# Kernel optimization log

Measured on AMD Instinct MI355X. Metric: run time of the kernel, lower is better.

## Reference

```python
import jax, jax.numpy as jnp
import numpy as np

EMBED = 768
HIDDEN = 3072
HEADS = 12
EPS = 1e-6


def _ln(x, g, b):
    mu = jnp.mean(x, axis=-1, keepdims=True)
    var = jnp.mean(jnp.square(x - mu), axis=-1, keepdims=True)
    return (x - mu) / jnp.sqrt(var + EPS) * g + b


def setup_inputs() -> dict:
    key = jax.random.key(0)
    ks = jax.random.split(key, 12)
    s = lambda fan_in: 1.0 / np.sqrt(fan_in)
    x = jax.random.normal(ks[0], (16, 1024, EMBED), dtype=jnp.float32)
    return {
        "x": x,
        "ln1_g": jnp.ones((EMBED,), jnp.float32),
        "ln1_b": jnp.zeros((EMBED,), jnp.float32),
        "qkv_w": jax.random.uniform(ks[1], (3 * EMBED, EMBED), jnp.float32, -s(EMBED), s(EMBED)),
        "qkv_b": jax.random.uniform(ks[2], (3 * EMBED,), jnp.float32, -s(EMBED), s(EMBED)),
        "proj_w": jax.random.uniform(ks[3], (EMBED, EMBED), jnp.float32, -s(EMBED), s(EMBED)),
        "proj_b": jax.random.uniform(ks[4], (EMBED,), jnp.float32, -s(EMBED), s(EMBED)),
        "ln2_g": jnp.ones((EMBED,), jnp.float32),
        "ln2_b": jnp.zeros((EMBED,), jnp.float32),
        "fc1_w": jax.random.uniform(ks[5], (HIDDEN, EMBED), jnp.float32, -s(EMBED), s(EMBED)),
        "fc1_b": jax.random.uniform(ks[6], (HIDDEN,), jnp.float32, -s(EMBED), s(EMBED)),
        "fc2_w": jax.random.uniform(ks[7], (EMBED, HIDDEN), jnp.float32, -s(HIDDEN), s(HIDDEN)),
        "fc2_b": jax.random.uniform(ks[8], (EMBED,), jnp.float32, -s(HIDDEN), s(HIDDEN)),
    }


def reference(x, ln1_g, ln1_b, qkv_w, qkv_b, proj_w, proj_b, ln2_g, ln2_b, fc1_w, fc1_b, fc2_w, fc2_b):
    B, N, D = x.shape
    Hd = D // HEADS
    scale = Hd ** -0.5
    # attention branch
    xn = _ln(x, ln1_g, ln1_b)
    qkv = xn @ qkv_w.T + qkv_b  # [B,N,3D]
    qkv = qkv.reshape(B, N, 3, HEADS, Hd).transpose(2, 0, 3, 1, 4)
    q, k, v = qkv[0], qkv[1], qkv[2]  # [B,H,N,Hd]
    attn = jax.nn.softmax(jnp.einsum("bhqd,bhkd->bhqk", q, k) * scale, axis=-1)
    ctx = jnp.einsum("bhqk,bhkd->bhqd", attn, v)
    ctx = ctx.transpose(0, 2, 1, 3).reshape(B, N, D)
    x = x + ctx @ proj_w.T + proj_b
    # MLP branch
    h = _ln(x, ln2_g, ln2_b)
    h = jax.nn.gelu(h @ fc1_w.T + fc1_b, approximate=False)
    x = x + h @ fc2_w.T + fc2_b
    return x
```

## Files before the change

kernel.cpp:

```cpp
#include <hip/hip_runtime.h>
#include <math.h>


typedef unsigned short u16;
typedef __attribute__((ext_vector_type(8))) short bf16x8;
typedef __attribute__((ext_vector_type(4))) float f32x4;

#define MFMA_BF16(a, b, c) __builtin_amdgcn_mfma_f32_16x16x32_bf16((a), (b), (c), 0, 0, 0)
#define MEMFENCE asm volatile("" ::: "memory")
#define WAITV(N) asm volatile("s_waitcnt vmcnt(" #N ")" ::: "memory")
#define WAITLGKM0 asm volatile("s_waitcnt lgkmcnt(0)" ::: "memory")
#define SCHED0 __builtin_amdgcn_sched_barrier(0)
#define EXP2F(x) __builtin_amdgcn_exp2f(x)

#define QSCALE 0.18033688011112042f
#define C8LOG2E 11.541560327111707f

__device__ __forceinline__ float bf2f(u16 v) {
    return __uint_as_float(((unsigned)v) << 16);
}
__device__ __forceinline__ u16 f2bf(float f) {
    unsigned u = __float_as_uint(f);
    u += 0x7fffu + ((u >> 16) & 1u);
    return (u16)(u >> 16);
}
__device__ __forceinline__ unsigned cvtpk_bf16(float lo, float hi) {
    unsigned r;
    asm volatile("v_cvt_pk_bf16_f32 %0, %1, %2" : "=v"(r) : "v"(lo), "v"(hi));
    return r;
}

__device__ __forceinline__ float gelu_fast(float v) {
    const float t = v * v;
    const float z = v * (1.5957691216f + 0.0713548162f * t);
    const float e = __expf(-z);
    return v * __builtin_amdgcn_rcpf(1.0f + e);
}

typedef __attribute__((address_space(1))) const void gvoid;
typedef __attribute__((address_space(3))) void lvoid;
__device__ __forceinline__ void gll16(const void* g, void* l) {
    __builtin_amdgcn_global_load_lds((gvoid*)g, (lvoid*)l, 16, 0, 0);
}

__global__ __launch_bounds__(256) void cast32(const float* __restrict__ src,
                                              u16* __restrict__ dst, int n8) {
    const int i = blockIdx.x * 256 + threadIdx.x;
    if (i >= n8) return;
    const float4 a = ((const float4*)src)[2 * i];
    const float4 b = ((const float4*)src)[2 * i + 1];
    bf16x8 r;
    r[0] = (short)f2bf(a.x); r[1] = (short)f2bf(a.y);
    r[2] = (short)f2bf(a.z); r[3] = (short)f2bf(a.w);
    r[4] = (short)f2bf(b.x); r[5] = (short)f2bf(b.y);
    r[6] = (short)f2bf(b.z); r[7] = (short)f2bf(b.w);
    ((bf16x8*)dst)[i] = r;
}

__global__ __launch_bounds__(256) void ln_kernel(const float* __restrict__ x,
                                                 const float* __restrict__ g,
                                                 const float* __restrict__ b,
                                                 u16* __restrict__ out) {
    const int row = blockIdx.x;
    const int t = threadIdx.x;
    const float* xr = x + (size_t)row * 768;
    float v0 = xr[t], v1 = xr[t + 256], v2 = xr[t + 512];
    float s = v0 + v1 + v2;
    float sq = v0 * v0 + v1 * v1 + v2 * v2;
#pragma unroll
    for (int off = 32; off > 0; off >>= 1) {
        s += __shfl_down(s, off);
        sq += __shfl_down(sq, off);
    }
    __shared__ float red_s[4], red_sq[4], sh_mu, sh_rs;
    const int wave = t >> 6, lane = t & 63;
    if (lane == 0) { red_s[wave] = s; red_sq[wave] = sq; }
    __syncthreads();
    if (t == 0) {
        float S = red_s[0] + red_s[1] + red_s[2] + red_s[3];
        float SQ = red_sq[0] + red_sq[1] + red_sq[2] + red_sq[3];
        float mu = S * (1.0f / 768.0f);
        float var = SQ * (1.0f / 768.0f) - mu * mu;
        sh_mu = mu;
        sh_rs = 1.0f / sqrtf(fmaxf(var, 0.0f) + 1e-6f);
    }
    __syncthreads();
    const float mu = sh_mu, rs = sh_rs;
    u16* orow = out + (size_t)row * 768;
    orow[t]       = f2bf((v0 - mu) * rs * g[t]       + b[t]);
    orow[t + 256] = f2bf((v1 - mu) * rs * g[t + 256] + b[t + 256]);
    orow[t + 512] = f2bf((v2 - mu) * rs * g[t + 512] + b[t + 512]);
}

template <int EPI, int BF16B>
__global__ __launch_bounds__(256, 2) void gemm2(
        const u16* __restrict__ A, const void* __restrict__ Bv,
        const float* __restrict__ bias, const float* __restrict__ res,
        void* __restrict__ Cv, u16* __restrict__ vtb, int N, int K) {
    __shared__ __align__(16) u16 As[128 * 32];
    __shared__ __align__(16) u16 Bs[128 * 32];
    const int t = threadIdx.x;
    const int wave = t >> 6, lane = t & 63;
    const int quad = lane >> 4, mr = lane & 15;
    const int wm = wave >> 1, wn = wave & 1;
    const int m0 = blockIdx.y * 128;
    const int n0 = blockIdx.x * 128;

    f32x4 acc[4][4];
#pragma unroll
    for (int i = 0; i < 4; i++)
#pragma unroll
        for (int j = 0; j < 4; j++) acc[i][j] = (f32x4){0.f, 0.f, 0.f, 0.f};

    const int seg = wave * 2;
    const int drow = lane >> 2;
    const int dcol = (lane & 3) * 8;
    const int sr = t >> 2, skv = t & 3;

    for (int k0 = 0; k0 < K; k0 += 32) {
#pragma unroll
        for (int c = 0; c < 2; c++) {
            const int rowA = (seg + c) * 16 + drow;
            gll16(A + (size_t)(m0 + rowA) * K + k0 + dcol, &As[(seg + c) * 512]);
        }
        if (BF16B) {
            const u16* Bh = (const u16*)Bv;
#pragma unroll
            for (int c = 0; c < 2; c++) {
                const int rowB = (seg + c) * 16 + drow;
                gll16(Bh + (size_t)(n0 + rowB) * K + k0 + dcol, &Bs[(seg + c) * 512]);
            }
        } else {
            const float* Bf = (const float*)Bv;
#pragma unroll
            for (int half = 0; half < 2; half++) {
                const float* src = Bf + (size_t)(n0 + sr + half * 64) * K + k0 + skv * 8;
                const float4 a = *(const float4*)src;
                const float4 b2 = *(const float4*)(src + 4);
                bf16x8 r;
                r[0] = (short)f2bf(a.x);  r[1] = (short)f2bf(a.y);
                r[2] = (short)f2bf(a.z);  r[3] = (short)f2bf(a.w);
                r[4] = (short)f2bf(b2.x); r[5] = (short)f2bf(b2.y);
                r[6] = (short)f2bf(b2.z); r[7] = (short)f2bf(b2.w);
                *(bf16x8*)&Bs[(sr + half * 64) * 32 + skv * 8] = r;
            }
        }
        __syncthreads();
        bf16x8 af[4], bfr[4];
#pragma unroll
        for (int i = 0; i < 4; i++)
            af[i] = *(const bf16x8*)&As[(wm * 64 + i * 16 + mr) * 32 + quad * 8];
#pragma unroll
        for (int j = 0; j < 4; j++)
            bfr[j] = *(const bf16x8*)&Bs[(wn * 64 + j * 16 + mr) * 32 + quad * 8];
#pragma unroll
        for (int i = 0; i < 4; i++)
#pragma unroll
            for (int j = 0; j < 4; j++)
                acc[i][j] = MFMA_BF16(af[i], bfr[j], acc[i][j]);
        __syncthreads();
    }

#pragma unroll
    for (int i = 0; i < 4; i++) {
#pragma unroll
        for (int r = 0; r < 4; r++) {
            const int m = m0 + wm * 64 + i * 16 + quad * 4 + r;
#pragma unroll
            for (int j = 0; j < 4; j++) {
                const int n = n0 + wn * 64 + j * 16 + mr;
                float v = acc[i][j][r] + bias[n];
                if (EPI == 1) {
                    v = gelu_fast(v);
                    ((u16*)Cv)[(size_t)m * N + n] = f2bf(v);
                } else if (EPI == 2) {
                    v += res[(size_t)m * N + n];
                    ((float*)Cv)[(size_t)m * N + n] = v;
                } else {
                    if (n < 1536) {
                        const float vq = (n < 768) ? v * QSCALE : v;
                        ((u16*)Cv)[(size_t)m * 1536 + n] = f2bf(vq);
                    } else {
                        const int h = (n - 1536) >> 6, hd = (n - 1536) & 63;
                        const int bb = m >> 10, pos = m & 1023;
                        vtb[((size_t)(bb * 12 + h) * 64 + hd) * 1024 + pos] = f2bf(v);
                    }
                }
            }
        }
    }
}

#define AFRAG(T, ROW, KS) \
    (*(const bf16x8*)&(T)[(ROW)][(((((KS) << 2) | quad)) ^ ((ROW) & 7)) << 3])

#define ACCUM(ACCEL, AF, BF)                                  \
    do {                                                      \
        if (EPI == 3) (ACCEL) = MFMA_BF16((AF), (BF), (ACCEL)); \
        else          (ACCEL) = MFMA_BF16((BF), (AF), (ACCEL)); \
    } while (0)

template <int EPI>
__global__ __launch_bounds__(512, 2) void gemm8(
        const u16* __restrict__ A, const u16* __restrict__ Bw,
        const float* __restrict__ bias, const float* __restrict__ res,
        void* __restrict__ Cv, u16* __restrict__ vtb, int N, int K) {
    __shared__ __align__(16) u16 SMEM[4][256][64];
    u16(&As)[2][256][64] = *reinterpret_cast<u16(*)[2][256][64]>(&SMEM[0][0][0]);
    u16(&Bs)[2][256][64] = *reinterpret_cast<u16(*)[2][256][64]>(&SMEM[2][0][0]);
    const int t = threadIdx.x;
    const int wave = t >> 6, lane = t & 63;
    const int quad = lane >> 4, mr = lane & 15;
    const int wm = wave >> 2, wn = wave & 3;
    const int gx = gridDim.x;
    const int nwg = gx * gridDim.y;
    int bid = blockIdx.y * gx + blockIdx.x;
    bid = (bid & 7) * (nwg >> 3) + (bid >> 3);
    const int m0 = (bid / gx) * 256, n0 = (bid % gx) * 256;
    const int NT = K >> 6;

    const int srow = wave * 8 + (lane >> 3);
    const int sgrp = ((lane & 7) ^ (lane >> 3)) * 8;

    const u16* Abase = A + (size_t)(m0 + srow) * K + sgrp;
    const u16* Bbase = Bw + (size_t)(n0 + srow) * K + sgrp;

#define STAGE_A(BI, SLOT, KT) \
    gll16(Abase + ((size_t)(SLOT) * 64) * K + (KT) * 64, &As[BI][(SLOT) * 64 + wave * 8][0])
#define STAGE_B(BI, SLOT, KT) \
    gll16(Bbase + ((size_t)(SLOT) * 64) * K + (KT) * 64, &Bs[BI][(SLOT) * 64 + wave * 8][0])

    STAGE_A(0, 0, 0); STAGE_A(0, 1, 0); STAGE_A(0, 2, 0); STAGE_A(0, 3, 0);
    STAGE_B(0, 0, 0); STAGE_B(0, 1, 0); STAGE_B(0, 2, 0); STAGE_B(0, 3, 0);
    if (NT > 1) { STAGE_A(1, 0, 1); STAGE_A(1, 2, 1); STAGE_B(1, 0, 1); STAGE_B(1, 1, 1); }

    f32x4 acc[8][4];
#pragma unroll
    for (int i = 0; i < 8; i++)
#pragma unroll
        for (int j = 0; j < 4; j++) acc[i][j] = (f32x4){0.f, 0.f, 0.f, 0.f};

    if (NT > 1) { WAITV(4); } else { WAITV(0); }
    __builtin_amdgcn_s_barrier();
    SCHED0;

    for (int kt = 0; kt < NT; ++kt) {
        const int bi = kt & 1;
        const u16(*Ab)[64] = As[bi];
        const u16(*Bb)[64] = Bs[bi];
        const bool st1 = (kt + 1 < NT);
        const bool st2 = (kt + 2 < NT);

        if (st1) { STAGE_B(bi ^ 1, 2, kt + 1); STAGE_B(bi ^ 1, 3, kt + 1);
                   STAGE_A(bi ^ 1, 1, kt + 1); STAGE_A(bi ^ 1, 3, kt + 1); }

        bf16x8 af[4], bfv[4];
#pragma unroll
        for (int j = 0; j < 4; j++) bfv[j] = AFRAG(Bb, wn * 64 + j * 16 + mr, 0);
#pragma unroll
        for (int i = 0; i < 4; i++) af[i] = AFRAG(Ab, wm * 128 + i * 16 + mr, 0);
#pragma unroll
        for (int i = 0; i < 4; i++)
#pragma unroll
            for (int j = 0; j < 4; j++) ACCUM(acc[i][j], af[i], bfv[j]);
#pragma unroll
        for (int i = 0; i < 4; i++) af[i] = AFRAG(Ab, wm * 128 + 64 + i * 16 + mr, 0);
#pragma unroll
        for (int i = 0; i < 4; i++)
#pragma unroll
            for (int j = 0; j < 4; j++) ACCUM(acc[4 + i][j], af[i], bfv[j]);
#pragma unroll
        for (int j = 0; j < 4; j++) bfv[j] = AFRAG(Bb, wn * 64 + j * 16 + mr, 1);
#pragma unroll
        for (int i = 0; i < 4; i++) af[i] = AFRAG(Ab, wm * 128 + i * 16 + mr, 1);
#pragma unroll
        for (int i = 0; i < 4; i++)
#pragma unroll
            for (int j = 0; j < 4; j++) ACCUM(acc[i][j], af[i], bfv[j]);
#pragma unroll
        for (int i = 0; i < 4; i++) af[i] = AFRAG(Ab, wm * 128 + 64 + i * 16 + mr, 1);
#pragma unroll
        for (int i = 0; i < 4; i++)
#pragma unroll
            for (int j = 0; j < 4; j++) ACCUM(acc[4 + i][j], af[i], bfv[j]);

        WAITLGKM0;
        SCHED0;
        __builtin_amdgcn_s_barrier();
        SCHED0;
        if (st2) { STAGE_A(bi, 0, kt + 2); STAGE_A(bi, 2, kt + 2);
                   STAGE_B(bi, 0, kt + 2); STAGE_B(bi, 1, kt + 2); }
        SCHED0;
        if (st2) { WAITV(4); } else { WAITV(0); }
        __builtin_amdgcn_s_barrier();
        SCHED0;
    }

    if (EPI == 3) {
        if (n0 >= 1536) {
            u16* Ls = &SMEM[0][0][0];
            __syncthreads();
#pragma unroll
            for (int i = 0; i < 8; i++) {
                const int mbase = wm * 128 + i * 16 + quad * 4;
                const int mch = mbase >> 3, mlo = mbase & 7;
#pragma unroll
                for (int j = 0; j < 4; j++) {
                    const int nl = wn * 64 + j * 16 + mr;
                    float v0 = acc[i][j][0] + bias[n0 + nl];
                    float v1 = acc[i][j][1] + bias[n0 + nl];
                    float v2 = acc[i][j][2] + bias[n0 + nl];
                    float v3 = acc[i][j][3] + bias[n0 + nl];
                    ushort4 w;
                    w.x = f2bf(v0); w.y = f2bf(v1); w.z = f2bf(v2); w.w = f2bf(v3);
                    *(ushort4*)(Ls + nl * 256 + ((mch ^ (nl & 7)) << 3) + mlo) = w;
                }
            }
            __syncthreads();
            const int bb = m0 >> 10, pos0 = m0 & 1023;
#pragma unroll
            for (int it = 0; it < 32; it++) {
                const int nl = it * 8 + wave;
                const int h = (n0 - 1536 + nl) >> 6;
                const int hd = nl & 63;
                const int mch = (lane >> 1) ^ (nl & 7);
                const ushort4 v =
                    *(const ushort4*)(Ls + nl * 256 + (mch << 3) + (lane & 1) * 4);
                u16* dst = vtb + ((size_t)(bb * 12 + h) * 64 + hd) * 1024 + pos0 + lane * 4;
                *(ushort4*)dst = v;
            }
        } else {
#pragma unroll
            for (int i = 0; i < 8; i++) {
#pragma unroll
                for (int r = 0; r < 4; r++) {
                    const int m = m0 + wm * 128 + (i >> 2) * 64 + (i & 3) * 16 + quad * 4 + r;
#pragma unroll
                    for (int j = 0; j < 4; j++) {
                        const int n = n0 + wn * 64 + j * 16 + mr;
                        float v = acc[i][j][r] + bias[n];
                        const float vq = (n < 768) ? v * QSCALE : v;
                        ((u16*)Cv)[(size_t)m * 1536 + n] = f2bf(vq);
                    }
                }
            }
        }
    } else {
#pragma unroll
        for (int ii = 0; ii < 8; ii++) {
            const int m = m0 + wm * 128 + (ii >> 2) * 64 + (ii & 3) * 16 + mr;
#pragma unroll
            for (int j = 0; j < 4; j++) {
                const int n = n0 + wn * 64 + j * 16 + quad * 4;
                const float4 b4 = *(const float4*)&bias[n];
                const float v0 = acc[ii][j][0] + b4.x;
                const float v1 = acc[ii][j][1] + b4.y;
                const float v2 = acc[ii][j][2] + b4.z;
                const float v3 = acc[ii][j][3] + b4.w;
                if (EPI == 1) {
                    ushort4 w;
                    w.x = f2bf(gelu_fast(v0)); w.y = f2bf(gelu_fast(v1));
                    w.z = f2bf(gelu_fast(v2)); w.w = f2bf(gelu_fast(v3));
                    *(ushort4*)&((u16*)Cv)[(size_t)m * N + n] = w;
                } else {
                    const float4 r4 = *(const float4*)&res[(size_t)m * N + n];
                    float4 o;
                    o.x = v0 + r4.x; o.y = v1 + r4.y; o.z = v2 + r4.z; o.w = v3 + r4.w;
                    *(float4*)&((float*)Cv)[(size_t)m * N + n] = o;
                }
            }
        }
    }
#undef STAGE_A
#undef STAGE_B
}

__global__ __launch_bounds__(256) void attn2(const u16* __restrict__ qkkb,
                                             const u16* __restrict__ vtb,
                                             u16* __restrict__ ctx) {
    __shared__ __align__(16) u16 Ks[2][64][72];
    __shared__ __align__(16) u16 Vt[2][64][72];
    __shared__ __align__(16) u16 Ps[64][72];
    const int L = blockIdx.y * gridDim.x + blockIdx.x;
    const int lxcd = L & 7, li = L >> 3;
    const int bh = lxcd * 24 + (li >> 4);
    const int q0 = (li & 15) * 64;
    const int b = bh / 12, h = bh % 12;
    const int t = threadIdx.x;
    const int wave = t >> 6, lane = t & 63, quad = lane >> 4, mr = lane & 15;

    const u16* qrow = qkkb + (size_t)(b * 1024 + q0 + wave * 16 + mr) * 1536 + h * 64;
    const bf16x8 qf0 = *(const bf16x8*)(qrow + quad * 8);
    const bf16x8 qf1 = *(const bf16x8*)(qrow + 32 + quad * 8);

    const u16* kbase = qkkb + (size_t)b * 1024 * 1536 + 768 + h * 64;
    const u16* vbase = vtb + (size_t)bh * 64 * 1024;

    const int srow = t >> 3;
    const int sv = t & 7;

    f32x4 oacc[4];
#pragma unroll
    for (int j = 0; j < 4; j++) oacc[j] = (f32x4){0.f, 0.f, 0.f, 0.f};
    float lsum = 0.f;

    bf16x8 pk0, pk1, pv0, pv1;
    pk0 = *(const bf16x8*)(kbase + (size_t)(srow)      * 1536 + sv * 8);
    pk1 = *(const bf16x8*)(kbase + (size_t)(srow + 32) * 1536 + sv * 8);
    pv0 = *(const bf16x8*)(vbase + (size_t)(srow)      * 1024 + sv * 8);
    pv1 = *(const bf16x8*)(vbase + (size_t)(srow + 32) * 1024 + sv * 8);
    *(bf16x8*)&Ks[0][srow][sv * 8] = pk0;
    *(bf16x8*)&Ks[0][srow + 32][sv * 8] = pk1;
    *(bf16x8*)&Vt[0][srow][sv * 8] = pv0;
    *(bf16x8*)&Vt[0][srow + 32][sv * 8] = pv1;

    for (int kt = 0; kt < 16; ++kt) {
        __syncthreads();
        const int cur = kt & 1;
        if (kt < 15) {
            const size_t ko = (size_t)(kt + 1) * 64;
            pk0 = *(const bf16x8*)(kbase + (ko + srow)      * 1536 + sv * 8);
            pk1 = *(const bf16x8*)(kbase + (ko + srow + 32) * 1536 + sv * 8);
            pv0 = *(const bf16x8*)(vbase + (size_t)(srow)      * 1024 + ko + sv * 8);
            pv1 = *(const bf16x8*)(vbase + (size_t)(srow + 32) * 1024 + ko + sv * 8);
        }
        f32x4 sf[4];
#pragma unroll
        for (int j = 0; j < 4; j++) {
            const bf16x8 kf0 = *(const bf16x8*)&Ks[cur][j * 16 + mr][quad * 8];
            const bf16x8 kf1 = *(const bf16x8*)&Ks[cur][j * 16 + mr][32 + quad * 8];
            f32x4 s = (f32x4){0.f, 0.f, 0.f, 0.f};
            s = MFMA_BF16(kf0, qf0, s);
            s = MFMA_BF16(kf1, qf1, s);
            sf[j] = s;
        }
#pragma unroll
        for (int j = 0; j < 4; j++) {
            const float p0 = EXP2F(sf[j][0] - C8LOG2E);
            const float p1 = EXP2F(sf[j][1] - C8LOG2E);
            const float p2 = EXP2F(sf[j][2] - C8LOG2E);
            const float p3 = EXP2F(sf[j][3] - C8LOG2E);
            lsum += (p0 + p1) + (p2 + p3);
            uint2 w;
            w.x = cvtpk_bf16(p0, p1);
            w.y = cvtpk_bf16(p2, p3);
            *(uint2*)&Ps[wave * 16 + mr][j * 16 + quad * 4] = w;
        }
        __asm__ __volatile__("s_waitcnt lgkmcnt(0)" ::: "memory");
#pragma unroll
        for (int st = 0; st < 2; st++) {
            const bf16x8 pf = *(const bf16x8*)&Ps[wave * 16 + mr][st * 32 + quad * 8];
#pragma unroll
            for (int j = 0; j < 4; j++) {
                const bf16x8 vf = *(const bf16x8*)&Vt[cur][j * 16 + mr][st * 32 + quad * 8];
                oacc[j] = MFMA_BF16(vf, pf, oacc[j]);
            }
        }
        if (kt < 15) {
            const int nxt = cur ^ 1;
            *(bf16x8*)&Ks[nxt][srow][sv * 8] = pk0;
            *(bf16x8*)&Ks[nxt][srow + 32][sv * 8] = pk1;
            *(bf16x8*)&Vt[nxt][srow][sv * 8] = pv0;
            *(bf16x8*)&Vt[nxt][srow + 32][sv * 8] = pv1;
        }
    }

    lsum += __shfl_xor(lsum, 16);
    lsum += __shfl_xor(lsum, 32);
    const float inv = 1.0f / lsum;
    u16* dst = ctx + (size_t)(b * 1024 + q0 + wave * 16 + mr) * 768 + h * 64;
#pragma unroll
    for (int j = 0; j < 4; j++) {
        ushort4 w;
        w.x = f2bf(oacc[j][0] * inv);
        w.y = f2bf(oacc[j][1] * inv);
        w.z = f2bf(oacc[j][2] * inv);
        w.w = f2bf(oacc[j][3] * inv);
        *(ushort4*)(dst + j * 16 + quad * 4) = w;
    }
}

extern "C" void kernel_launch(void* const* d_in, const int* in_sizes, int n_in,
                              void* d_out, int out_size, void* d_ws, size_t ws_size,
                              hipStream_t stream) {
    const float* x      = (const float*)d_in[0];
    const float* ln1_g  = (const float*)d_in[1];
    const float* ln1_b  = (const float*)d_in[2];
    const float* qkv_w  = (const float*)d_in[3];
    const float* qkv_b  = (const float*)d_in[4];
    const float* proj_w = (const float*)d_in[5];
    const float* proj_b = (const float*)d_in[6];
    const float* ln2_g  = (const float*)d_in[7];
    const float* ln2_b  = (const float*)d_in[8];
    const float* fc1_w  = (const float*)d_in[9];
    const float* fc1_b  = (const float*)d_in[10];
    const float* fc2_w  = (const float*)d_in[11];
    const float* fc2_b  = (const float*)d_in[12];
    float* out = (float*)d_out;

    char* base = (char*)d_ws + 1024;
    u16* xn   = (u16*)base;
    u16* qkkb = (u16*)(base + 25165824);
    u16* vtb  = (u16*)(base + 75497472);
    u16* h1   = (u16*)(base + 25165824);
    u16* ctxb = xn;
    u16* hn   = xn;

    const size_t WOFF = 125830144ull;
    const bool big = ws_size >= 139985920ull;
    u16* wqkv  = (u16*)((char*)d_ws + WOFF);
    u16* wproj = (u16*)((char*)d_ws + WOFF + 3538944);
    u16* wfc1  = (u16*)((char*)d_ws + WOFF + 4718592);
    u16* wfc2  = (u16*)((char*)d_ws + WOFF + 9437184);

    if (big) {
        cast32<<<dim3(864),  dim3(256), 0, stream>>>(qkv_w,  wqkv,  221184);
        cast32<<<dim3(288),  dim3(256), 0, stream>>>(proj_w, wproj, 73728);
        cast32<<<dim3(1152), dim3(256), 0, stream>>>(fc1_w,  wfc1,  294912);
        cast32<<<dim3(1152), dim3(256), 0, stream>>>(fc2_w,  wfc2,  294912);
    }

    ln_kernel<<<dim3(16384), dim3(256), 0, stream>>>(x, ln1_g, ln1_b, xn);

    if (big)
        gemm8<3><<<dim3(9, 64), dim3(512), 0, stream>>>(
            xn, wqkv, qkv_b, nullptr, qkkb, vtb, 2304, 768);
    else
        gemm2<3, 0><<<dim3(18, 128), dim3(256), 0, stream>>>(
            xn, qkv_w, qkv_b, nullptr, qkkb, vtb, 2304, 768);

    attn2<<<dim3(16, 192), dim3(256), 0, stream>>>(qkkb, vtb, ctxb);

    if (big)
        gemm8<2><<<dim3(3, 64), dim3(512), 0, stream>>>(
            ctxb, wproj, proj_b, x, out, nullptr, 768, 768);
    else
        gemm2<2, 0><<<dim3(6, 128), dim3(256), 0, stream>>>(
            ctxb, proj_w, proj_b, x, out, nullptr, 768, 768);

    ln_kernel<<<dim3(16384), dim3(256), 0, stream>>>(out, ln2_g, ln2_b, hn);

    if (big)
        gemm8<1><<<dim3(12, 64), dim3(512), 0, stream>>>(
            hn, wfc1, fc1_b, nullptr, h1, nullptr, 3072, 768);
    else
        gemm2<1, 0><<<dim3(24, 128), dim3(256), 0, stream>>>(
            hn, fc1_w, fc1_b, nullptr, h1, nullptr, 3072, 768);

    if (big)
        gemm8<2><<<dim3(3, 64), dim3(512), 0, stream>>>(
            h1, wfc2, fc2_b, out, out, nullptr, 768, 3072);
    else
        gemm2<2, 0><<<dim3(6, 128), dim3(256), 0, stream>>>(
            h1, fc2_w, fc2_b, out, out, nullptr, 768, 3072);
}
```

Baseline: 563.8 us.

## Restructure GEMM main loop into eight-phase ping-pong with setprio and split stages

Replaces the per-k-tile GEMM loop with a two-tile unrolled loop split into eight phases. Each phase loads a quadrant of A/B fragments, issues part of the next global-to-LDS staging, and runs 16 MFMAs bracketed by s_setprio, with barriers between phases. The aim is to interleave memory staging with MFMA work more finely and let waves alternate priority so compute and loads overlap. It assumes NT is even and at least 2, and adds more barriers per k-tile.

Result: no change. 555.3 us (-1.5%).

```diff
diff --git a/kernel.cpp b/kernel.cpp
--- a/kernel.cpp
+++ b/kernel.cpp
@@ -7,7 +7,6 @@
 typedef __attribute__((ext_vector_type(4))) float f32x4;
 
 #define MFMA_BF16(a, b, c) __builtin_amdgcn_mfma_f32_16x16x32_bf16((a), (b), (c), 0, 0, 0)
-#define MEMFENCE asm volatile("" ::: "memory")
 #define WAITV(N) asm volatile("s_waitcnt vmcnt(" #N ")" ::: "memory")
 #define WAITLGKM0 asm volatile("s_waitcnt lgkmcnt(0)" ::: "memory")
 #define SCHED0 __builtin_amdgcn_sched_barrier(0)
@@ -200,6 +199,40 @@
         else          (ACCEL) = MFMA_BF16((BF), (AF), (ACCEL)); \
     } while (0)
 
+#define PHASE(BI, RH, CH, DO_RA, DO_RB, STAGES, WAITS)                          \
+    do {                                                                        \
+        if (DO_RA) {                                                            \
+            _Pragma("unroll") for (int rb = 0; rb < 4; rb++)                    \
+                _Pragma("unroll") for (int kk = 0; kk < 2; kk++)                \
+                    af[rb * 2 + kk] =                                           \
+                        AFRAG(As[BI], wm * 128 + (RH) * 64 + rb * 16 + mr, kk); \
+        }                                                                       \
+        if (DO_RB) {                                                            \
+            _Pragma("unroll") for (int cb = 0; cb < 2; cb++)                    \
+                _Pragma("unroll") for (int kk = 0; kk < 2; kk++)                \
+                    bc[CH][cb * 2 + kk] =                                       \
+                        AFRAG(Bs[BI], wn * 64 + (CH) * 32 + cb * 16 + mr, kk);  \
+        }                                                                       \
+        STAGES;                                                                 \
+        SCHED0;                                                                 \
+        __builtin_amdgcn_s_barrier();                                           \
+        WAITLGKM0;                                                              \
+        SCHED0;                                                                 \
+        __builtin_amdgcn_s_setprio(1);                                          \
+        _Pragma("unroll") for (int rb = 0; rb < 4; rb++)                        \
+            _Pragma("unroll") for (int cb = 0; cb < 2; cb++) {                  \
+                ACCUM(acc[(RH) * 4 + rb][(CH) * 2 + cb], af[rb * 2 + 0],        \
+                      bc[CH][cb * 2 + 0]);                                      \
+                ACCUM(acc[(RH) * 4 + rb][(CH) * 2 + cb], af[rb * 2 + 1],        \
+                      bc[CH][cb * 2 + 1]);                                      \
+            }                                                                   \
+        __builtin_amdgcn_s_setprio(0);                                          \
+        SCHED0;                                                                 \
+        WAITS;                                                                  \
+        __builtin_amdgcn_s_barrier();                                           \
+        SCHED0;                                                                 \
+    } while (0)
+
 template <int EPI>
 __global__ __launch_bounds__(512, 2) void gemm8(
         const u16* __restrict__ A, const u16* __restrict__ Bw,
@@ -218,6 +251,7 @@
     bid = (bid & 7) * (nwg >> 3) + (bid >> 3);
     const int m0 = (bid / gx) * 256, n0 = (bid % gx) * 256;
     const int NT = K >> 6;
+    const int NI = NT >> 1;
 
     const int srow = wave * 8 + (lane >> 3);
     const int sgrp = ((lane & 7) ^ (lane >> 3)) * 8;
@@ -232,7 +266,8 @@
 
     STAGE_A(0, 0, 0); STAGE_A(0, 1, 0); STAGE_A(0, 2, 0); STAGE_A(0, 3, 0);
     STAGE_B(0, 0, 0); STAGE_B(0, 1, 0); STAGE_B(0, 2, 0); STAGE_B(0, 3, 0);
-    if (NT > 1) { STAGE_A(1, 0, 1); STAGE_A(1, 2, 1); STAGE_B(1, 0, 1); STAGE_B(1, 1, 1); }
+    STAGE_A(1, 0, 1); STAGE_A(1, 1, 1); STAGE_A(1, 2, 1); STAGE_A(1, 3, 1);
+    STAGE_B(1, 0, 1); STAGE_B(1, 1, 1); STAGE_B(1, 2, 1); STAGE_B(1, 3, 1);
 
     f32x4 acc[8][4];
 #pragma unroll
@@ -240,60 +275,37 @@
 #pragma unroll
         for (int j = 0; j < 4; j++) acc[i][j] = (f32x4){0.f, 0.f, 0.f, 0.f};
 
-    if (NT > 1) { WAITV(4); } else { WAITV(0); }
+    WAITV(8);
     __builtin_amdgcn_s_barrier();
     SCHED0;
 
-    for (int kt = 0; kt < NT; ++kt) {
-        const int bi = kt & 1;
-        const u16(*Ab)[64] = As[bi];
-        const u16(*Bb)[64] = Bs[bi];
-        const bool st1 = (kt + 1 < NT);
-        const bool st2 = (kt + 2 < NT);
-
-        if (st1) { STAGE_B(bi ^ 1, 2, kt + 1); STAGE_B(bi ^ 1, 3, kt + 1);
-                   STAGE_A(bi ^ 1, 1, kt + 1); STAGE_A(bi ^ 1, 3, kt + 1); }
-
-        bf16x8 af[4], bfv[4];
-#pragma unroll
-        for (int j = 0; j < 4; j++) bfv[j] = AFRAG(Bb, wn * 64 + j * 16 + mr, 0);
-#pragma unroll
-        for (int i = 0; i < 4; i++) af[i] = AFRAG(Ab, wm * 128 + i * 16 + mr, 0);
-#pragma unroll
-        for (int i = 0; i < 4; i++)
-#pragma unroll
-            for (int j = 0; j < 4; j++) ACCUM(acc[i][j], af[i], bfv[j]);
-#pragma unroll
-        for (int i = 0; i < 4; i++) af[i] = AFRAG(Ab, wm * 128 + 64 + i * 16 + mr, 0);
-#pragma unroll
-        for (int i = 0; i < 4; i++)
-#pragma unroll
-            for (int j = 0; j < 4; j++) ACCUM(acc[4 + i][j], af[i], bfv[j]);
-#pragma unroll
-        for (int j = 0; j < 4; j++) bfv[j] = AFRAG(Bb, wn * 64 + j * 16 + mr, 1);
-#pragma unroll
-        for (int i = 0; i < 4; i++) af[i] = AFRAG(Ab, wm * 128 + i * 16 + mr, 1);
-#pragma unroll
-        for (int i = 0; i < 4; i++)
-#pragma unroll
-            for (int j = 0; j < 4; j++) ACCUM(acc[i][j], af[i], bfv[j]);
-#pragma unroll
-        for (int i = 0; i < 4; i++) af[i] = AFRAG(Ab, wm * 128 + 64 + i * 16 + mr, 1);
-#pragma unroll
-        for (int i = 0; i < 4; i++)
-#pragma unroll
-            for (int j = 0; j < 4; j++) ACCUM(acc[4 + i][j], af[i], bfv[j]);
-
-        WAITLGKM0;
-        SCHED0;
-        __builtin_amdgcn_s_barrier();
-        SCHED0;
-        if (st2) { STAGE_A(bi, 0, kt + 2); STAGE_A(bi, 2, kt + 2);
-                   STAGE_B(bi, 0, kt + 2); STAGE_B(bi, 1, kt + 2); }
-        SCHED0;
-        if (st2) { WAITV(4); } else { WAITV(0); }
-        __builtin_amdgcn_s_barrier();
-        SCHED0;
+    bf16x8 af[8], bc[2][4];
+
+    for (int it = 0; it < NI; ++it) {
+        const int ka = it * 2;
+        const int kb = ka + 1;
+        const bool s2 = (ka + 2 < NT);
+        const bool s3 = (ka + 3 < NT);
+
+        PHASE(0, 0, 0, 1, 1,
+              { if (it) { STAGE_A(1, 0, kb); STAGE_A(1, 1, kb); } }, {});
+        PHASE(0, 0, 1, 0, 1,
+              { if (it) { STAGE_A(1, 2, kb); STAGE_A(1, 3, kb); } }, {});
+        PHASE(0, 1, 1, 1, 0,
+              { if (s2) { STAGE_B(0, 0, ka + 2); STAGE_B(0, 1, ka + 2); } }, {});
+        PHASE(0, 1, 0, 0, 0,
+              { if (s2) { STAGE_B(0, 2, ka + 2); STAGE_B(0, 3, ka + 2); } },
+              { if (s2) { WAITV(4); } else { WAITV(0); } });
+
+        PHASE(1, 0, 0, 1, 1,
+              { if (s2) { STAGE_A(0, 0, ka + 2); STAGE_A(0, 1, ka + 2); } }, {});
+        PHASE(1, 0, 1, 0, 1,
+              { if (s2) { STAGE_A(0, 2, ka + 2); STAGE_A(0, 3, ka + 2); } }, {});
+        PHASE(1, 1, 1, 1, 0,
+              { if (s3) { STAGE_B(1, 0, ka + 3); STAGE_B(1, 1, ka + 3); } }, {});
+        PHASE(1, 1, 0, 0, 0,
+              { if (s3) { STAGE_B(1, 2, ka + 3); STAGE_B(1, 3, ka + 3); } },
+              { if (s3) { WAITV(4); } else { WAITV(0); } });
     }
 
     if (EPI == 3) {
@@ -302,7 +314,7 @@
             __syncthreads();
 #pragma unroll
             for (int i = 0; i < 8; i++) {
-                const int mbase = wm * 128 + i * 16 + quad * 4;
+                const int mbase = wm * 128 + (i >> 2) * 64 + (i & 3) * 16 + quad * 4;
                 const int mch = mbase >> 3, mlo = mbase & 7;
 #pragma unroll
                 for (int j = 0; j < 4; j++) {
@@ -319,8 +331,8 @@
             __syncthreads();
             const int bb = m0 >> 10, pos0 = m0 & 1023;
 #pragma unroll
-            for (int it = 0; it < 32; it++) {
-                const int nl = it * 8 + wave;
+            for (int it2 = 0; it2 < 32; it2++) {
+                const int nl = it2 * 8 + wave;
                 const int h = (n0 - 1536 + nl) >> 6;
                 const int hd = nl & 63;
                 const int mch = (lane >> 1) ^ (nl & 7);
```
